# Kernel tuning notes

Hardware: AMD Instinct MI355X
Metric: run time of the kernel (lower is better)

## Reference

```python
import jax, jax.numpy as jnp
import numpy as np

BALL_SIZE = 128


def setup_inputs() -> dict:
    key = jax.random.key(0)
    kq, kk, kv = jax.random.split(key, 3)
    B, H, n, Dh = 4, 16, 8192, 64
    q = jax.random.normal(kq, (B, H, n, Dh), dtype=jnp.float32)
    k = jax.random.normal(kk, (B, H, n, Dh), dtype=jnp.float32)
    v = jax.random.normal(kv, (B, H, n, Dh), dtype=jnp.float32)
    return {"q": q, "k": k, "v": v}


def reference(q, k, v) -> jnp.ndarray:
    # Block-local (ball) attention: attention computed independently within
    # each contiguous ball of size BALL_SIZE along the sequence dim.
    B, H, n, Dh = q.shape
    bs = BALL_SIZE
    m = n // bs
    # (B, H, m, bs, D) -- split seq into balls; attention only within a ball.
    qb = q.reshape(B, H, m, bs, Dh)
    kb = k.reshape(B, H, m, bs, Dh)
    vb = v.reshape(B, H, m, bs, Dh)
    scale = 1.0 / jnp.sqrt(jnp.asarray(Dh, dtype=q.dtype))
    scores = jnp.einsum('bhmqd,bhmkd->bhmqk', qb, kb) * scale  # (B,H,m,bs,bs)
    attn = jax.nn.softmax(scores, axis=-1)
    out = jnp.einsum('bhmqk,bhmkd->bhmqd', attn, vb)
    return out.reshape(B, H, n, Dh)
```

## Files before the change

### kernel.cpp

```cpp
#include <hip/hip_runtime.h>

typedef _Float16 half2_t __attribute__((ext_vector_type(2)));
typedef _Float16 half4_t __attribute__((ext_vector_type(4)));
typedef _Float16 half8_t __attribute__((ext_vector_type(8)));
typedef __fp16   fp16x2  __attribute__((ext_vector_type(2)));
typedef float    f32x4   __attribute__((ext_vector_type(4)));

#define BS 128
#define DH 64

__device__ __forceinline__ half2_t pkrtz(float x, float y) {
  fp16x2 t = __builtin_amdgcn_cvt_pkrtz(x, y);
  return __builtin_bit_cast(half2_t, t);
}

__device__ __forceinline__ half4_t cvt4(const float4 a) {
  half2_t h0 = pkrtz(a.x, a.y);
  half2_t h1 = pkrtz(a.z, a.w);
  return __builtin_shufflevector(h0, h1, 0, 1, 2, 3);
}

__device__ __forceinline__ half8_t cvt8(const float4 a, const float4 b) {
  half2_t h0 = pkrtz(a.x, a.y);
  half2_t h1 = pkrtz(a.z, a.w);
  half2_t h2 = pkrtz(b.x, b.y);
  half2_t h3 = pkrtz(b.z, b.w);
  half4_t lo = __builtin_shufflevector(h0, h1, 0, 1, 2, 3);
  half4_t hi = __builtin_shufflevector(h2, h3, 0, 1, 2, 3);
  return __builtin_shufflevector(lo, hi, 0, 1, 2, 3, 4, 5, 6, 7);
}

__global__ __launch_bounds__(256, 1) void ball_attn_kernel(
    const float* __restrict__ Q, const float* __restrict__ Kk,
    const float* __restrict__ V, float* __restrict__ O) {
  __shared__ __align__(16) _Float16 Kh[BS * DH];
  __shared__ __align__(16) _Float16 VT[DH * BS];
  __shared__ __align__(16) _Float16 Pl[4 * 16 * BS];

  const int tid  = threadIdx.x;
  const int w    = tid >> 6;
  const int lane = tid & 63;
  const int c    = lane & 15;
  const int g    = lane >> 4;

  const size_t base = (size_t)blockIdx.x * (BS * DH);
  const float* Qb = Q + base;
  const float* Kb = Kk + base;
  const float* Vb = V + base;
  float*       Ob = O + base;

  const int d0   = (tid & 15) * 4;
  const int kgrp = tid >> 4;
  float4 vA[4], vB[4], kA[4], kB[4];
#pragma unroll
  for (int it = 0; it < 4; ++it) {
    const int keyA = 2 * kgrp + 32 * it;
    vA[it] = *(const float4*)(Vb + (size_t)keyA * DH + d0);
    vB[it] = *(const float4*)(Vb + (size_t)(keyA + 1) * DH + d0);
    kA[it] = *(const float4*)(Kb + (size_t)keyA * DH + d0);
    kB[it] = *(const float4*)(Kb + (size_t)(keyA + 1) * DH + d0);
  }
#pragma unroll
  for (int it = 0; it < 4; ++it) {
    const int keyA = 2 * kgrp + 32 * it;
    *(half4_t*)&Kh[keyA * DH + (d0 ^ ((keyA & 7) << 3))]           = cvt4(kA[it]);
    *(half4_t*)&Kh[(keyA + 1) * DH + (d0 ^ (((keyA + 1) & 7) << 3))] = cvt4(kB[it]);
    const float* ap = (const float*)&vA[it];
    const float* bp = (const float*)&vB[it];
#pragma unroll
    for (int j = 0; j < 4; ++j) {
      const int d = d0 + j;
      *(half2_t*)&VT[d * BS + (keyA ^ (((d >> 2) & 7) << 3))] = pkrtz(ap[j], bp[j]);
    }
  }

  half8_t aq[2][2];
#pragma unroll
  for (int m = 0; m < 2; ++m)
#pragma unroll
    for (int ks = 0; ks < 2; ++ks) {
      const float* qp = Qb + (w * 32 + m * 16 + c) * DH + ks * 32 + g * 8;
      aq[m][ks] = cvt8(*(const float4*)qp, *(const float4*)(qp + 4));
    }

  __syncthreads();

  f32x4 acc[2][8];
#pragma unroll
  for (int m = 0; m < 2; ++m)
#pragma unroll
    for (int kt = 0; kt < 8; ++kt) acc[m][kt] = (f32x4){0.f, 0.f, 0.f, 0.f};

#pragma unroll
  for (int kt = 0; kt < 8; ++kt)
#pragma unroll
    for (int ks = 0; ks < 2; ++ks) {
      const half8_t bk =
          *(const half8_t*)&Kh[(kt * 16 + c) * DH + ((ks * 32 + g * 8) ^ ((c & 7) << 3))];
      acc[0][kt] = __builtin_amdgcn_mfma_f32_16x16x32_f16(aq[0][ks], bk, acc[0][kt], 0, 0, 0);
      acc[1][kt] = __builtin_amdgcn_mfma_f32_16x16x32_f16(aq[1][ks], bk, acc[1][kt], 0, 0, 0);
    }

#pragma unroll
  for (int m = 0; m < 2; ++m) {
    float mx[4], sm[4], inv[4];
#pragma unroll
    for (int r = 0; r < 4; ++r) {
      mx[r] = acc[m][0][r];
#pragma unroll
      for (int kt = 1; kt < 8; ++kt) mx[r] = fmaxf(mx[r], acc[m][kt][r]);
    }
#pragma unroll
    for (int r = 0; r < 4; ++r) {
      mx[r] = fmaxf(mx[r], __shfl_xor(mx[r], 1));
      mx[r] = fmaxf(mx[r], __shfl_xor(mx[r], 2));
      mx[r] = fmaxf(mx[r], __shfl_xor(mx[r], 4));
      mx[r] = fmaxf(mx[r], __shfl_xor(mx[r], 8));
      sm[r] = 0.f;
    }
#pragma unroll
    for (int kt = 0; kt < 8; ++kt)
#pragma unroll
      for (int r = 0; r < 4; ++r) {
        const float p = __expf((acc[m][kt][r] - mx[r]) * 0.125f);
        acc[m][kt][r] = p;
        sm[r] += p;
      }
#pragma unroll
    for (int r = 0; r < 4; ++r) {
      sm[r] += __shfl_xor(sm[r], 1);
      sm[r] += __shfl_xor(sm[r], 2);
      sm[r] += __shfl_xor(sm[r], 4);
      sm[r] += __shfl_xor(sm[r], 8);
      inv[r] = __builtin_amdgcn_rcpf(sm[r]);
    }
#pragma unroll
    for (int kt = 0; kt < 8; ++kt)
#pragma unroll
      for (int r = 0; r < 4; ++r) {
        const int row = 4 * g + r;
        Pl[(w * 16 + row) * BS + ((kt * 16 + c) ^ ((row & 7) << 3))] =
            (_Float16)acc[m][kt][r];
      }

    f32x4 o[4];
#pragma unroll
    for (int t = 0; t < 4; ++t) o[t] = (f32x4){0.f, 0.f, 0.f, 0.f};
#pragma unroll
    for (int ks = 0; ks < 4; ++ks) {
      const int e0 = ks * 32 + g * 8;
      const half8_t pf = *(const half8_t*)&Pl[(w * 16 + c) * BS + (e0 ^ ((c & 7) << 3))];
#pragma unroll
      for (int t = 0; t < 4; ++t) {
        const int row = t * 16 + c;
        const half8_t vf = *(const half8_t*)&VT[row * BS + (e0 ^ (((row >> 2) & 7) << 3))];
        o[t] = __builtin_amdgcn_mfma_f32_16x16x32_f16(pf, vf, o[t], 0, 0, 0);
      }
    }
#pragma unroll
    for (int t = 0; t < 4; ++t)
#pragma unroll
      for (int r = 0; r < 4; ++r)
        Ob[(w * 32 + m * 16 + 4 * g + r) * DH + t * 16 + c] = o[t][r] * inv[r];
  }
}

extern "C" void kernel_launch(void* const* d_in, const int* in_sizes, int n_in,
                              void* d_out, int out_size, void* d_ws, size_t ws_size,
                              hipStream_t stream) {
  const float* q = (const float*)d_in[0];
  const float* k = (const float*)d_in[1];
  const float* v = (const float*)d_in[2];
  float* out = (float*)d_out;
  const int nballs = in_sizes[0] / (BS * DH);
  ball_attn_kernel<<<dim3(nballs), dim3(256), 0, stream>>>(q, k, v, out);
}
```

Measured before the change: 115.0 us.

## Make ball-attention kernel persistent over 8 balls with async K prefetch

Each block now processes 8 consecutive balls. The next ball's K is prefetched straight into LDS in fp32 via global_load_lds, and V and Q are loaded into registers while the current ball's softmax and PV run. V goes into a double-buffered transposed fp16 tile, and K is converted to fp16 at fragment load time. This hides global-load latency behind compute and changes the V swizzle. The cost is far fewer blocks (512 instead of 4096, fewer than the CU count times occupancy can use), extra syncs and doubled K LDS footprint.

```diff
diff --git a/kernel.cpp b/kernel.cpp
--- a/kernel.cpp
+++ b/kernel.cpp
@@ -8,16 +8,11 @@
 
 #define BS 128
 #define DH 64
+#define NB 8
 
 __device__ __forceinline__ half2_t pkrtz(float x, float y) {
   fp16x2 t = __builtin_amdgcn_cvt_pkrtz(x, y);
   return __builtin_bit_cast(half2_t, t);
-}
-
-__device__ __forceinline__ half4_t cvt4(const float4 a) {
-  half2_t h0 = pkrtz(a.x, a.y);
-  half2_t h1 = pkrtz(a.z, a.w);
-  return __builtin_shufflevector(h0, h1, 0, 1, 2, 3);
 }
 
 __device__ __forceinline__ half8_t cvt8(const float4 a, const float4 b) {
@@ -30,11 +25,13 @@
   return __builtin_shufflevector(lo, hi, 0, 1, 2, 3, 4, 5, 6, 7);
 }
 
+__device__ __forceinline__ int svt(int d) { return (d & 7) ^ ((d >> 2) & 7); }
+
 __global__ __launch_bounds__(256, 1) void ball_attn_kernel(
     const float* __restrict__ Q, const float* __restrict__ Kk,
     const float* __restrict__ V, float* __restrict__ O) {
-  __shared__ __align__(16) _Float16 Kh[BS * DH];
-  __shared__ __align__(16) _Float16 VT[DH * BS];
+  __shared__ __align__(16) float    Kf[BS * DH];
+  __shared__ __align__(16) _Float16 VT2[2][DH * BS];
   __shared__ __align__(16) _Float16 Pl[4 * 16 * BS];
 
   const int tid  = threadIdx.x;
@@ -42,126 +39,242 @@
   const int lane = tid & 63;
   const int c    = lane & 15;
   const int g    = lane >> 4;
-
-  const size_t base = (size_t)blockIdx.x * (BS * DH);
-  const float* Qb = Q + base;
-  const float* Kb = Kk + base;
-  const float* Vb = V + base;
-  float*       Ob = O + base;
-
   const int d0   = (tid & 15) * 4;
   const int kgrp = tid >> 4;
-  float4 vA[4], vB[4], kA[4], kB[4];
-#pragma unroll
-  for (int it = 0; it < 4; ++it) {
-    const int keyA = 2 * kgrp + 32 * it;
-    vA[it] = *(const float4*)(Vb + (size_t)keyA * DH + d0);
-    vB[it] = *(const float4*)(Vb + (size_t)(keyA + 1) * DH + d0);
-    kA[it] = *(const float4*)(Kb + (size_t)keyA * DH + d0);
-    kB[it] = *(const float4*)(Kb + (size_t)(keyA + 1) * DH + d0);
+
+  const size_t ball0 = (size_t)blockIdx.x * NB;
+
+  auto issueK = [&](const float* Kb) {
+#pragma unroll
+    for (int t = 0; t < 8; ++t) {
+      const int row = 32 * w + 4 * t + g;
+      const int u   = (lane & 15) ^ (row & 7);
+      __builtin_amdgcn_global_load_lds(
+          (const __attribute__((address_space(1))) unsigned int*)(Kb + row * DH + u * 4),
+          (__attribute__((address_space(3))) unsigned int*)&Kf[(32 * w + 4 * t) * DH],
+          16, 0, 0);
+    }
+  };
+  auto loadV = [&](const float* Vb, float4* vr) {
+#pragma unroll
+    for (int it = 0; it < 4; ++it) {
+      const int keyA = 2 * kgrp + 32 * it;
+      vr[2 * it]     = *(const float4*)(Vb + (size_t)keyA * DH + d0);
+      vr[2 * it + 1] = *(const float4*)(Vb + (size_t)(keyA + 1) * DH + d0);
+    }
+  };
+  auto writeVT = [&](_Float16* vt, const float4* vr) {
+#pragma unroll
+    for (int it = 0; it < 4; ++it) {
+      const int keyA = 2 * kgrp + 32 * it;
+      const float* ap = (const float*)&vr[2 * it];
+      const float* bp = (const float*)&vr[2 * it + 1];
+#pragma unroll
+      for (int j = 0; j < 4; ++j) {
+        const int d = d0 + j;
+        *(half2_t*)&vt[d * BS + (keyA ^ (svt(d) << 3))] = pkrtz(ap[j], bp[j]);
+      }
+    }
+  };
+  auto loadQ = [&](const float* Qb, float4* qr) {
+#pragma unroll
+    for (int m = 0; m < 2; ++m)
+#pragma unroll
+      for (int ks = 0; ks < 2; ++ks) {
+        const float* qp = Qb + (w * 32 + m * 16 + c) * DH + ks * 32 + g * 8;
+        qr[(m * 2 + ks) * 2]     = *(const float4*)qp;
+        qr[(m * 2 + ks) * 2 + 1] = *(const float4*)(qp + 4);
+      }
+  };
+
+  half8_t aq[2][2];
+  auto cvtQ = [&](const float4* qr) {
+#pragma unroll
+    for (int m = 0; m < 2; ++m)
+#pragma unroll
+      for (int ks = 0; ks < 2; ++ks)
+        aq[m][ks] = cvt8(qr[(m * 2 + ks) * 2], qr[(m * 2 + ks) * 2 + 1]);
+  };
+
+  {
+    const size_t b_off = ball0 * (size_t)(BS * DH);
+    issueK(Kk + b_off);
+    float4 vr[8], qr[8];
+    loadV(V + b_off, vr);
+    loadQ(Q + b_off, qr);
+    cvtQ(qr);
+    writeVT(VT2[0], vr);
+    __syncthreads();
   }
-#pragma unroll
-  for (int it = 0; it < 4; ++it) {
-    const int keyA = 2 * kgrp + 32 * it;
-    *(half4_t*)&Kh[keyA * DH + (d0 ^ ((keyA & 7) << 3))]           = cvt4(kA[it]);
-    *(half4_t*)&Kh[(keyA + 1) * DH + (d0 ^ (((keyA + 1) & 7) << 3))] = cvt4(kB[it]);
-    const float* ap = (const float*)&vA[it];
-    const float* bp = (const float*)&vB[it];
-#pragma unroll
-    for (int j = 0; j < 4; ++j) {
-      const int d = d0 + j;
-      *(half2_t*)&VT[d * BS + (keyA ^ (((d >> 2) & 7) << 3))] = pkrtz(ap[j], bp[j]);
-    }
-  }
-
-  half8_t aq[2][2];
-#pragma unroll
-  for (int m = 0; m < 2; ++m)
-#pragma unroll
-    for (int ks = 0; ks < 2; ++ks) {
-      const float* qp = Qb + (w * 32 + m * 16 + c) * DH + ks * 32 + g * 8;
-      aq[m][ks] = cvt8(*(const float4*)qp, *(const float4*)(qp + 4));
-    }
-
-  __syncthreads();
-
-  f32x4 acc[2][8];
-#pragma unroll
-  for (int m = 0; m < 2; ++m)
-#pragma unroll
-    for (int kt = 0; kt < 8; ++kt) acc[m][kt] = (f32x4){0.f, 0.f, 0.f, 0.f};
-
-#pragma unroll
-  for (int kt = 0; kt < 8; ++kt)
-#pragma unroll
-    for (int ks = 0; ks < 2; ++ks) {
-      const half8_t bk =
-          *(const half8_t*)&Kh[(kt * 16 + c) * DH + ((ks * 32 + g * 8) ^ ((c & 7) << 3))];
-      acc[0][kt] = __builtin_amdgcn_mfma_f32_16x16x32_f16(aq[0][ks], bk, acc[0][kt], 0, 0, 0);
-      acc[1][kt] = __builtin_amdgcn_mfma_f32_16x16x32_f16(aq[1][ks], bk, acc[1][kt], 0, 0, 0);
-    }
-
-#pragma unroll
-  for (int m = 0; m < 2; ++m) {
-    float mx[4], sm[4], inv[4];
-#pragma unroll
-    for (int r = 0; r < 4; ++r) {
-      mx[r] = acc[m][0][r];
-#pragma unroll
-      for (int kt = 1; kt < 8; ++kt) mx[r] = fmaxf(mx[r], acc[m][kt][r]);
-    }
-#pragma unroll
-    for (int r = 0; r < 4; ++r) {
-      mx[r] = fmaxf(mx[r], __shfl_xor(mx[r], 1));
-      mx[r] = fmaxf(mx[r], __shfl_xor(mx[r], 2));
-      mx[r] = fmaxf(mx[r], __shfl_xor(mx[r], 4));
-      mx[r] = fmaxf(mx[r], __shfl_xor(mx[r], 8));
-      sm[r] = 0.f;
-    }
+
+  int cur = 0;
+#pragma unroll 1
+  for (int i = 0; i < NB; ++i) {
+    _Float16* vtcur = VT2[cur];
+    float* Ob = O + (ball0 + i) * (size_t)(BS * DH);
+
+    f32x4 acc[2][8];
+#pragma unroll
+    for (int m = 0; m < 2; ++m)
+#pragma unroll
+      for (int kt = 0; kt < 8; ++kt) acc[m][kt] = (f32x4){0.f, 0.f, 0.f, 0.f};
 #pragma unroll
     for (int kt = 0; kt < 8; ++kt)
 #pragma unroll
-      for (int r = 0; r < 4; ++r) {
-        const float p = __expf((acc[m][kt][r] - mx[r]) * 0.125f);
-        acc[m][kt][r] = p;
-        sm[r] += p;
-      }
-#pragma unroll
-    for (int r = 0; r < 4; ++r) {
-      sm[r] += __shfl_xor(sm[r], 1);
-      sm[r] += __shfl_xor(sm[r], 2);
-      sm[r] += __shfl_xor(sm[r], 4);
-      sm[r] += __shfl_xor(sm[r], 8);
-      inv[r] = __builtin_amdgcn_rcpf(sm[r]);
-    }
-#pragma unroll
-    for (int kt = 0; kt < 8; ++kt)
-#pragma unroll
-      for (int r = 0; r < 4; ++r) {
-        const int row = 4 * g + r;
-        Pl[(w * 16 + row) * BS + ((kt * 16 + c) ^ ((row & 7) << 3))] =
-            (_Float16)acc[m][kt][r];
-      }
-
-    f32x4 o[4];
-#pragma unroll
-    for (int t = 0; t < 4; ++t) o[t] = (f32x4){0.f, 0.f, 0.f, 0.f};
-#pragma unroll
-    for (int ks = 0; ks < 4; ++ks) {
-      const int e0 = ks * 32 + g * 8;
-      const half8_t pf = *(const half8_t*)&Pl[(w * 16 + c) * BS + (e0 ^ ((c & 7) << 3))];
-#pragma unroll
-      for (int t = 0; t < 4; ++t) {
-        const int row = t * 16 + c;
-        const half8_t vf = *(const half8_t*)&VT[row * BS + (e0 ^ (((row >> 2) & 7) << 3))];
-        o[t] = __builtin_amdgcn_mfma_f32_16x16x32_f16(pf, vf, o[t], 0, 0, 0);
-      }
-    }
-#pragma unroll
-    for (int t = 0; t < 4; ++t)
-#pragma unroll
-      for (int r = 0; r < 4; ++r)
-        Ob[(w * 32 + m * 16 + 4 * g + r) * DH + t * 16 + c] = o[t][r] * inv[r];
+      for (int ks = 0; ks < 2; ++ks) {
+        const int row = kt * 16 + c;
+        const int sr  = row & 7;
+        const int u0  = 8 * ks + 2 * g;
+        const float4 a = *(const float4*)&Kf[row * DH + ((u0 ^ sr) * 4)];
+        const float4 b = *(const float4*)&Kf[row * DH + (((u0 + 1) ^ sr) * 4)];
+        const half8_t bk = cvt8(a, b);
+        acc[0][kt] = __builtin_amdgcn_mfma_f32_16x16x32_f16(aq[0][ks], bk, acc[0][kt], 0, 0, 0);
+        acc[1][kt] = __builtin_amdgcn_mfma_f32_16x16x32_f16(aq[1][ks], bk, acc[1][kt], 0, 0, 0);
+      }
+    __syncthreads();
+
+    const bool pf = (i + 1 < NB);
+    const size_t nb_off = (ball0 + i + 1) * (size_t)(BS * DH);
+    if (pf) issueK(Kk + nb_off);
+
+    float4 vraw[8], qraw[8];
+
+    float inv0[4];
+    {
+      float mx[4], sm[4];
+#pragma unroll
+      for (int r = 0; r < 4; ++r) {
+        mx[r] = acc[0][0][r];
+#pragma unroll
+        for (int kt = 1; kt < 8; ++kt) mx[r] = fmaxf(mx[r], acc[0][kt][r]);
+      }
+#pragma unroll
+      for (int r = 0; r < 4; ++r) {
+        mx[r] = fmaxf(mx[r], __shfl_xor(mx[r], 1));
+        mx[r] = fmaxf(mx[r], __shfl_xor(mx[r], 2));
+        mx[r] = fmaxf(mx[r], __shfl_xor(mx[r], 4));
+        mx[r] = fmaxf(mx[r], __shfl_xor(mx[r], 8));
+        sm[r] = 0.f;
+      }
+#pragma unroll
+      for (int kt = 0; kt < 8; ++kt)
+#pragma unroll
+        for (int r = 0; r < 4; ++r) {
+          const float p = __expf((acc[0][kt][r] - mx[r]) * 0.125f);
+          acc[0][kt][r] = p;
+          sm[r] += p;
+        }
+#pragma unroll
+      for (int r = 0; r < 4; ++r) {
+        sm[r] += __shfl_xor(sm[r], 1);
+        sm[r] += __shfl_xor(sm[r], 2);
+        sm[r] += __shfl_xor(sm[r], 4);
+        sm[r] += __shfl_xor(sm[r], 8);
+        inv0[r] = __builtin_amdgcn_rcpf(sm[r]);
+      }
+#pragma unroll
+      for (int kt = 0; kt < 8; ++kt)
+#pragma unroll
+        for (int r = 0; r < 4; ++r) {
+          const int row = 4 * g + r;
+          Pl[(w * 16 + row) * BS + ((kt * 16 + c) ^ ((row & 7) << 3))] =
+              (_Float16)acc[0][kt][r];
+        }
+    }
+    if (pf) loadV(V + nb_off, vraw);
+    {
+      f32x4 o[4];
+#pragma unroll
+      for (int t = 0; t < 4; ++t) o[t] = (f32x4){0.f, 0.f, 0.f, 0.f};
+#pragma unroll
+      for (int ks = 0; ks < 4; ++ks) {
+        const int e0 = ks * 32 + g * 8;
+        const half8_t pfg = *(const half8_t*)&Pl[(w * 16 + c) * BS + (e0 ^ ((c & 7) << 3))];
+#pragma unroll
+        for (int t = 0; t < 4; ++t) {
+          const int rowd = t * 16 + c;
+          const half8_t vf = *(const half8_t*)&vtcur[rowd * BS + (e0 ^ (svt(rowd) << 3))];
+          o[t] = __builtin_amdgcn_mfma_f32_16x16x32_f16(pfg, vf, o[t], 0, 0, 0);
+        }
+      }
+#pragma unroll
+      for (int t = 0; t < 4; ++t)
+#pragma unroll
+        for (int r = 0; r < 4; ++r)
+          Ob[(w * 32 + 4 * g + r) * DH + t * 16 + c] = o[t][r] * inv0[r];
+    }
+
+    float inv1[4];
+    {
+      float mx[4], sm[4];
+#pragma unroll
+      for (int r = 0; r < 4; ++r) {
+        mx[r] = acc[1][0][r];
+#pragma unroll
+        for (int kt = 1; kt < 8; ++kt) mx[r] = fmaxf(mx[r], acc[1][kt][r]);
+      }
+#pragma unroll
+      for (int r = 0; r < 4; ++r) {
+        mx[r] = fmaxf(mx[r], __shfl_xor(mx[r], 1));
+        mx[r] = fmaxf(mx[r], __shfl_xor(mx[r], 2));
+        mx[r] = fmaxf(mx[r], __shfl_xor(mx[r], 4));
+        mx[r] = fmaxf(mx[r], __shfl_xor(mx[r], 8));
+        sm[r] = 0.f;
+      }
+#pragma unroll
+      for (int kt = 0; kt < 8; ++kt)
+#pragma unroll
+        for (int r = 0; r < 4; ++r) {
+          const float p = __expf((acc[1][kt][r] - mx[r]) * 0.125f);
+          acc[1][kt][r] = p;
+          sm[r] += p;
+        }
+#pragma unroll
+      for (int r = 0; r < 4; ++r) {
+        sm[r] += __shfl_xor(sm[r], 1);
+        sm[r] += __shfl_xor(sm[r], 2);
+        sm[r] += __shfl_xor(sm[r], 4);
+        sm[r] += __shfl_xor(sm[r], 8);
+        inv1[r] = __builtin_amdgcn_rcpf(sm[r]);
+      }
+#pragma unroll
+      for (int kt = 0; kt < 8; ++kt)
+#pragma unroll
+        for (int r = 0; r < 4; ++r) {
+          const int row = 4 * g + r;
+          Pl[(w * 16 + row) * BS + ((kt * 16 + c) ^ ((row & 7) << 3))] =
+              (_Float16)acc[1][kt][r];
+        }
+    }
+    if (pf) loadQ(Q + nb_off, qraw);
+    {
+      f32x4 o[4];
+#pragma unroll
+      for (int t = 0; t < 4; ++t) o[t] = (f32x4){0.f, 0.f, 0.f, 0.f};
+#pragma unroll
+      for (int ks = 0; ks < 4; ++ks) {
+        const int e0 = ks * 32 + g * 8;
+        const half8_t pfg = *(const half8_t*)&Pl[(w * 16 + c) * BS + (e0 ^ ((c & 7) << 3))];
+#pragma unroll
+        for (int t = 0; t < 4; ++t) {
+          const int rowd = t * 16 + c;
+          const half8_t vf = *(const half8_t*)&vtcur[rowd * BS + (e0 ^ (svt(rowd) << 3))];
+          o[t] = __builtin_amdgcn_mfma_f32_16x16x32_f16(pfg, vf, o[t], 0, 0, 0);
+        }
+      }
+#pragma unroll
+      for (int t = 0; t < 4; ++t)
+#pragma unroll
+        for (int r = 0; r < 4; ++r)
+          Ob[(w * 32 + 16 + 4 * g + r) * DH + t * 16 + c] = o[t][r] * inv1[r];
+    }
+
+    if (pf) {
+      cvtQ(qraw);
+      writeVT(VT2[cur ^ 1], vraw);
+    }
+    __syncthreads();
+    cur ^= 1;
   }
 }
 
@@ -173,5 +286,5 @@
   const float* v = (const float*)d_in[2];
   float* out = (float*)d_out;
   const int nballs = in_sizes[0] / (BS * DH);
-  ball_attn_kernel<<<dim3(nballs), dim3(256), 0, stream>>>(q, k, v, out);
-}
+  ball_attn_kernel<<<dim3(nballs / NB), dim3(256), 0, stream>>>(q, k, v, out);
+}
```

Measured after the change: 125.7 us. 9.2% more time.

## Stream K fragments from global into registers, drop K LDS staging, remap blocks

Applied to the files above, without the earlier changes.

Removes the shared-memory K buffer. Each wave now loads its K fragments straight from global memory with a two-deep register prefetch and converts them to fp16 just before each MFMA. It also changes the VT swizzle to a new bank-conflict pattern, remaps block IDs to balls in an interleaved order, and drops the one-block-per-SM launch bound so smaller LDS use can allow more resident blocks. The intent is to cut LDS traffic and the staging cost, and to raise occupancy. In exchange, each of the four waves reads all of K from global/L2 separately, which adds redundant global loads.

```diff
diff --git a/kernel.cpp b/kernel.cpp
--- a/kernel.cpp
+++ b/kernel.cpp
@@ -14,12 +14,6 @@
   return __builtin_bit_cast(half2_t, t);
 }
 
-__device__ __forceinline__ half4_t cvt4(const float4 a) {
-  half2_t h0 = pkrtz(a.x, a.y);
-  half2_t h1 = pkrtz(a.z, a.w);
-  return __builtin_shufflevector(h0, h1, 0, 1, 2, 3);
-}
-
 __device__ __forceinline__ half8_t cvt8(const float4 a, const float4 b) {
   half2_t h0 = pkrtz(a.x, a.y);
   half2_t h1 = pkrtz(a.z, a.w);
@@ -30,10 +24,11 @@
   return __builtin_shufflevector(lo, hi, 0, 1, 2, 3, 4, 5, 6, 7);
 }
 
-__global__ __launch_bounds__(256, 1) void ball_attn_kernel(
+__device__ __forceinline__ int svt(int d) { return (d & 7) ^ ((d >> 2) & 7); }
+
+__global__ __launch_bounds__(256) void ball_attn_kernel(
     const float* __restrict__ Q, const float* __restrict__ Kk,
     const float* __restrict__ V, float* __restrict__ O) {
-  __shared__ __align__(16) _Float16 Kh[BS * DH];
   __shared__ __align__(16) _Float16 VT[DH * BS];
   __shared__ __align__(16) _Float16 Pl[4 * 16 * BS];
 
@@ -43,34 +38,36 @@
   const int c    = lane & 15;
   const int g    = lane >> 4;
 
-  const size_t base = (size_t)blockIdx.x * (BS * DH);
+  const int nwg  = gridDim.x;
+  const int bid  = blockIdx.x;
+  const int ball = (bid & 7) * (nwg >> 3) + (bid >> 3);
+
+  const size_t base = (size_t)ball * (BS * DH);
   const float* Qb = Q + base;
   const float* Kb = Kk + base;
   const float* Vb = V + base;
   float*       Ob = O + base;
 
-  const int d0   = (tid & 15) * 4;
-  const int kgrp = tid >> 4;
-  float4 vA[4], vB[4], kA[4], kB[4];
+  {
+    const int kgrp = tid >> 4;
+    const int d0   = (tid & 15) * 4;
+    float4 vA[4], vB[4];
 #pragma unroll
-  for (int it = 0; it < 4; ++it) {
-    const int keyA = 2 * kgrp + 32 * it;
-    vA[it] = *(const float4*)(Vb + (size_t)keyA * DH + d0);
-    vB[it] = *(const float4*)(Vb + (size_t)(keyA + 1) * DH + d0);
-    kA[it] = *(const float4*)(Kb + (size_t)keyA * DH + d0);
-    kB[it] = *(const float4*)(Kb + (size_t)(keyA + 1) * DH + d0);
-  }
+    for (int it = 0; it < 4; ++it) {
+      const int keyA = 2 * kgrp + 32 * it;
+      vA[it] = *(const float4*)(Vb + (size_t)keyA * DH + d0);
+      vB[it] = *(const float4*)(Vb + (size_t)(keyA + 1) * DH + d0);
+    }
 #pragma unroll
-  for (int it = 0; it < 4; ++it) {
-    const int keyA = 2 * kgrp + 32 * it;
-    *(half4_t*)&Kh[keyA * DH + (d0 ^ ((keyA & 7) << 3))]           = cvt4(kA[it]);
-    *(half4_t*)&Kh[(keyA + 1) * DH + (d0 ^ (((keyA + 1) & 7) << 3))] = cvt4(kB[it]);
-    const float* ap = (const float*)&vA[it];
-    const float* bp = (const float*)&vB[it];
+    for (int it = 0; it < 4; ++it) {
+      const int keyA = 2 * kgrp + 32 * it;
+      const float* ap = (const float*)&vA[it];
+      const float* bp = (const float*)&vB[it];
 #pragma unroll
-    for (int j = 0; j < 4; ++j) {
-      const int d = d0 + j;
-      *(half2_t*)&VT[d * BS + (keyA ^ (((d >> 2) & 7) << 3))] = pkrtz(ap[j], bp[j]);
+      for (int j = 0; j < 4; ++j) {
+        const int d = d0 + j;
+        *(half2_t*)&VT[d * BS + (keyA ^ (svt(d) << 3))] = pkrtz(ap[j], bp[j]);
+      }
     }
   }
 
@@ -91,15 +88,28 @@
 #pragma unroll
     for (int kt = 0; kt < 8; ++kt) acc[m][kt] = (f32x4){0.f, 0.f, 0.f, 0.f};
 
+  {
+    float4 kb[2][2];
+    auto kaddr = [&](int i) {
+      const int kt = i >> 1, ks = i & 1;
+      return Kb + (kt * 16 + c) * DH + ks * 32 + g * 8;
+    };
+    kb[0][0] = *(const float4*)kaddr(0);
+    kb[0][1] = *(const float4*)(kaddr(0) + 4);
+    kb[1][0] = *(const float4*)kaddr(1);
+    kb[1][1] = *(const float4*)(kaddr(1) + 4);
 #pragma unroll
-  for (int kt = 0; kt < 8; ++kt)
-#pragma unroll
-    for (int ks = 0; ks < 2; ++ks) {
-      const half8_t bk =
-          *(const half8_t*)&Kh[(kt * 16 + c) * DH + ((ks * 32 + g * 8) ^ ((c & 7) << 3))];
+    for (int i = 0; i < 16; ++i) {
+      const half8_t bk = cvt8(kb[i & 1][0], kb[i & 1][1]);
+      if (i + 2 < 16) {
+        kb[i & 1][0] = *(const float4*)kaddr(i + 2);
+        kb[i & 1][1] = *(const float4*)(kaddr(i + 2) + 4);
+      }
+      const int kt = i >> 1, ks = i & 1;
       acc[0][kt] = __builtin_amdgcn_mfma_f32_16x16x32_f16(aq[0][ks], bk, acc[0][kt], 0, 0, 0);
       acc[1][kt] = __builtin_amdgcn_mfma_f32_16x16x32_f16(aq[1][ks], bk, acc[1][kt], 0, 0, 0);
     }
+  }
 
 #pragma unroll
   for (int m = 0; m < 2; ++m) {
@@ -149,12 +159,12 @@
 #pragma unroll
     for (int ks = 0; ks < 4; ++ks) {
       const int e0 = ks * 32 + g * 8;
-      const half8_t pf = *(const half8_t*)&Pl[(w * 16 + c) * BS + (e0 ^ ((c & 7) << 3))];
+      const half8_t pfg = *(const half8_t*)&Pl[(w * 16 + c) * BS + (e0 ^ ((c & 7) << 3))];
 #pragma unroll
       for (int t = 0; t < 4; ++t) {
-        const int row = t * 16 + c;
-        const half8_t vf = *(const half8_t*)&VT[row * BS + (e0 ^ (((row >> 2) & 7) << 3))];
-        o[t] = __builtin_amdgcn_mfma_f32_16x16x32_f16(pf, vf, o[t], 0, 0, 0);
+        const int rowd = t * 16 + c;
+        const half8_t vf = *(const half8_t*)&VT[rowd * BS + (e0 ^ (svt(rowd) << 3))];
+        o[t] = __builtin_amdgcn_mfma_f32_16x16x32_f16(pfg, vf, o[t], 0, 0, 0);
       }
     }
 #pragma unroll
```

Result: slower. 131.6 us (+14.4%).

## Switch to 32x32 MFMA with transposed scores and register-resident P

Applied to the files above, without the earlier changes.

Recomputes S^T = K·Q^T using 32x32x16 MFMA so each lane holds a full query column, which lets the softmax reductions run within a lane plus one cross-half shuffle. K is read straight from global into MFMA operands, so the K shared-memory tile is gone. The P matrix is repacked in registers with permlane32 swaps instead of going through LDS. V^T staging uses a new swizzle and the launch-bounds occupancy hint is removed. The aim is to cut LDS traffic, LDS footprint and shuffle count. In exchange, each wave now loads K from global/L2 on its own, four times per block, and register pressure rises.

```diff
diff --git a/kernel.cpp b/kernel.cpp
--- a/kernel.cpp
+++ b/kernel.cpp
@@ -4,23 +4,21 @@
 typedef _Float16 half4_t __attribute__((ext_vector_type(4)));
 typedef _Float16 half8_t __attribute__((ext_vector_type(8)));
 typedef __fp16   fp16x2  __attribute__((ext_vector_type(2)));
-typedef float    f32x4   __attribute__((ext_vector_type(4)));
+typedef float    f32x16  __attribute__((ext_vector_type(16)));
 
 #define BS 128
 #define DH 64
 
-__device__ __forceinline__ half2_t pkrtz(float x, float y) {
+static __device__ __forceinline__ half2_t pkrtz(float x, float y) {
   fp16x2 t = __builtin_amdgcn_cvt_pkrtz(x, y);
   return __builtin_bit_cast(half2_t, t);
 }
-
-__device__ __forceinline__ half4_t cvt4(const float4 a) {
-  half2_t h0 = pkrtz(a.x, a.y);
-  half2_t h1 = pkrtz(a.z, a.w);
-  return __builtin_shufflevector(h0, h1, 0, 1, 2, 3);
+static __device__ __forceinline__ unsigned pkrtz_u(float x, float y) {
+  fp16x2 t = __builtin_amdgcn_cvt_pkrtz(x, y);
+  return __builtin_bit_cast(unsigned, t);
 }
 
-__device__ __forceinline__ half8_t cvt8(const float4 a, const float4 b) {
+static __device__ __forceinline__ half8_t cvt8(const float4 a, const float4 b) {
   half2_t h0 = pkrtz(a.x, a.y);
   half2_t h1 = pkrtz(a.z, a.w);
   half2_t h2 = pkrtz(b.x, b.y);
@@ -30,18 +28,46 @@
   return __builtin_shufflevector(lo, hi, 0, 1, 2, 3, 4, 5, 6, 7);
 }
 
-__global__ __launch_bounds__(256, 1) void ball_attn_kernel(
+static __device__ __forceinline__ half8_t h8_from(unsigned r0, unsigned r1,
+                                                  unsigned r2, unsigned r3) {
+  half2_t h0 = __builtin_bit_cast(half2_t, r0);
+  half2_t h1 = __builtin_bit_cast(half2_t, r1);
+  half2_t h2 = __builtin_bit_cast(half2_t, r2);
+  half2_t h3 = __builtin_bit_cast(half2_t, r3);
+  half4_t lo = __builtin_shufflevector(h0, h1, 0, 1, 2, 3);
+  half4_t hi = __builtin_shufflevector(h2, h3, 0, 1, 2, 3);
+  return __builtin_shufflevector(lo, hi, 0, 1, 2, 3, 4, 5, 6, 7);
+}
+
+static __device__ __forceinline__ void plswap(unsigned x, unsigned y,
+                                              unsigned& olo, unsigned& ohi) {
+#if __has_builtin(__builtin_amdgcn_permlane32_swap)
+  auto pr = __builtin_amdgcn_permlane32_swap((int)x, (int)y, false, false);
+  unsigned tmp[2];
+  __builtin_memcpy(tmp, &pr, 8);
+  olo = tmp[0];
+  ohi = tmp[1];
+#else
+  const int h = (threadIdx.x & 63) >> 5;
+  unsigned xs = (unsigned)__shfl_xor((int)x, 32);
+  unsigned ys = (unsigned)__shfl_xor((int)y, 32);
+  olo = h ? ys : x;
+  ohi = h ? y : xs;
+#endif
+}
+
+static __device__ __forceinline__ int svt(int d) { return (d & 7) ^ ((d >> 2) & 7); }
+
+__global__ __launch_bounds__(256) void ball_attn_kernel(
     const float* __restrict__ Q, const float* __restrict__ Kk,
     const float* __restrict__ V, float* __restrict__ O) {
-  __shared__ __align__(16) _Float16 Kh[BS * DH];
   __shared__ __align__(16) _Float16 VT[DH * BS];
-  __shared__ __align__(16) _Float16 Pl[4 * 16 * BS];
 
   const int tid  = threadIdx.x;
   const int w    = tid >> 6;
   const int lane = tid & 63;
-  const int c    = lane & 15;
-  const int g    = lane >> 4;
+  const int ld   = lane & 31;
+  const int hi   = lane >> 5;
 
   const size_t base = (size_t)blockIdx.x * (BS * DH);
   const float* Qb = Q + base;
@@ -49,120 +75,104 @@
   const float* Vb = V + base;
   float*       Ob = O + base;
 
-  const int d0   = (tid & 15) * 4;
-  const int kgrp = tid >> 4;
-  float4 vA[4], vB[4], kA[4], kB[4];
+  {
+    const int kgrp = tid >> 4;
+    const int d0   = (tid & 15) * 4;
+    float4 vA[4], vB[4];
 #pragma unroll
-  for (int it = 0; it < 4; ++it) {
-    const int keyA = 2 * kgrp + 32 * it;
-    vA[it] = *(const float4*)(Vb + (size_t)keyA * DH + d0);
-    vB[it] = *(const float4*)(Vb + (size_t)(keyA + 1) * DH + d0);
-    kA[it] = *(const float4*)(Kb + (size_t)keyA * DH + d0);
-    kB[it] = *(const float4*)(Kb + (size_t)(keyA + 1) * DH + d0);
-  }
+    for (int it = 0; it < 4; ++it) {
+      const int keyA = 2 * kgrp + 32 * it;
+      vA[it] = *(const float4*)(Vb + (size_t)keyA * DH + d0);
+      vB[it] = *(const float4*)(Vb + (size_t)(keyA + 1) * DH + d0);
+    }
 #pragma unroll
-  for (int it = 0; it < 4; ++it) {
-    const int keyA = 2 * kgrp + 32 * it;
-    *(half4_t*)&Kh[keyA * DH + (d0 ^ ((keyA & 7) << 3))]           = cvt4(kA[it]);
-    *(half4_t*)&Kh[(keyA + 1) * DH + (d0 ^ (((keyA + 1) & 7) << 3))] = cvt4(kB[it]);
-    const float* ap = (const float*)&vA[it];
-    const float* bp = (const float*)&vB[it];
+    for (int it = 0; it < 4; ++it) {
+      const int keyA = 2 * kgrp + 32 * it;
+      const float* ap = (const float*)&vA[it];
+      const float* bp = (const float*)&vB[it];
 #pragma unroll
-    for (int j = 0; j < 4; ++j) {
-      const int d = d0 + j;
-      *(half2_t*)&VT[d * BS + (keyA ^ (((d >> 2) & 7) << 3))] = pkrtz(ap[j], bp[j]);
+      for (int j = 0; j < 4; ++j) {
+        const int d = d0 + j;
+        *(half2_t*)&VT[d * BS + (keyA ^ (svt(d) << 3))] = pkrtz(ap[j], bp[j]);
+      }
     }
   }
 
-  half8_t aq[2][2];
+  half8_t bq[4];
 #pragma unroll
-  for (int m = 0; m < 2; ++m)
-#pragma unroll
-    for (int ks = 0; ks < 2; ++ks) {
-      const float* qp = Qb + (w * 32 + m * 16 + c) * DH + ks * 32 + g * 8;
-      aq[m][ks] = cvt8(*(const float4*)qp, *(const float4*)(qp + 4));
-    }
+  for (int dstep = 0; dstep < 4; ++dstep) {
+    const float* qp = Qb + (w * 32 + ld) * DH + dstep * 16 + hi * 8;
+    bq[dstep] = cvt8(*(const float4*)qp, *(const float4*)(qp + 4));
+  }
 
   __syncthreads();
 
-  f32x4 acc[2][8];
+  f32x16 acc[4] = {};
 #pragma unroll
-  for (int m = 0; m < 2; ++m)
+  for (int kt = 0; kt < 4; ++kt) {
+    const float* krow = Kb + (kt * 32 + ld) * DH + hi * 8;
 #pragma unroll
-    for (int kt = 0; kt < 8; ++kt) acc[m][kt] = (f32x4){0.f, 0.f, 0.f, 0.f};
+    for (int dstep = 0; dstep < 4; ++dstep) {
+      const float* kp = krow + dstep * 16;
+      const half8_t ak = cvt8(*(const float4*)kp, *(const float4*)(kp + 4));
+      acc[kt] = __builtin_amdgcn_mfma_f32_32x32x16_f16(ak, bq[dstep], acc[kt], 0, 0, 0);
+    }
+  }
+
+  float mx = acc[0][0];
+#pragma unroll
+  for (int kt = 0; kt < 4; ++kt)
+#pragma unroll
+    for (int r = 0; r < 16; ++r) mx = fmaxf(mx, acc[kt][r]);
+  mx = fmaxf(mx, __shfl_xor(mx, 32));
+  const float nmxs = -mx * 0.125f;
+  float sm = 0.f;
+#pragma unroll
+  for (int kt = 0; kt < 4; ++kt)
+#pragma unroll
+    for (int r = 0; r < 16; ++r) {
+      const float p = __expf(fmaf(acc[kt][r], 0.125f, nmxs));
+      acc[kt][r] = p;
+      sm += p;
+    }
+  sm += __shfl_xor(sm, 32);
+  const float inv = __builtin_amdgcn_rcpf(sm);
+
+  half8_t pf[8];
+#pragma unroll
+  for (int s = 0; s < 8; ++s) {
+    const int kt = s >> 1;
+    const int bA = 2 * (s & 1);
+    const int bB = bA + 1;
+    const unsigned A0 = pkrtz_u(acc[kt][4 * bA + 0] * inv, acc[kt][4 * bA + 1] * inv);
+    const unsigned A1 = pkrtz_u(acc[kt][4 * bA + 2] * inv, acc[kt][4 * bA + 3] * inv);
+    const unsigned B0 = pkrtz_u(acc[kt][4 * bB + 0] * inv, acc[kt][4 * bB + 1] * inv);
+    const unsigned B1 = pkrtz_u(acc[kt][4 * bB + 2] * inv, acc[kt][4 * bB + 3] * inv);
+    unsigned r0, r1, r2, r3;
+    plswap(A0, B0, r0, r2);
+    plswap(A1, B1, r1, r3);
+    pf[s] = h8_from(r0, r1, r2, r3);
+  }
+
+  f32x16 o[2] = {};
+#pragma unroll
+  for (int dt = 0; dt < 2; ++dt) {
+    const int row = dt * 32 + ld;
+    const int sv  = svt(row) << 3;
+#pragma unroll
+    for (int s = 0; s < 8; ++s) {
+      const half8_t vf = *(const half8_t*)&VT[row * BS + ((16 * s + 8 * hi) ^ sv)];
+      o[dt] = __builtin_amdgcn_mfma_f32_32x32x16_f16(pf[s], vf, o[dt], 0, 0, 0);
+    }
+  }
 
 #pragma unroll
-  for (int kt = 0; kt < 8; ++kt)
+  for (int dt = 0; dt < 2; ++dt)
 #pragma unroll
-    for (int ks = 0; ks < 2; ++ks) {
-      const half8_t bk =
-          *(const half8_t*)&Kh[(kt * 16 + c) * DH + ((ks * 32 + g * 8) ^ ((c & 7) << 3))];
-      acc[0][kt] = __builtin_amdgcn_mfma_f32_16x16x32_f16(aq[0][ks], bk, acc[0][kt], 0, 0, 0);
-      acc[1][kt] = __builtin_amdgcn_mfma_f32_16x16x32_f16(aq[1][ks], bk, acc[1][kt], 0, 0, 0);
+    for (int r = 0; r < 16; ++r) {
+      const int qrow = w * 32 + (r & 3) + 8 * (r >> 2) + 4 * hi;
+      Ob[qrow * DH + dt * 32 + ld] = o[dt][r];
     }
-
-#pragma unroll
-  for (int m = 0; m < 2; ++m) {
-    float mx[4], sm[4], inv[4];
-#pragma unroll
-    for (int r = 0; r < 4; ++r) {
-      mx[r] = acc[m][0][r];
-#pragma unroll
-      for (int kt = 1; kt < 8; ++kt) mx[r] = fmaxf(mx[r], acc[m][kt][r]);
-    }
-#pragma unroll
-    for (int r = 0; r < 4; ++r) {
-      mx[r] = fmaxf(mx[r], __shfl_xor(mx[r], 1));
-      mx[r] = fmaxf(mx[r], __shfl_xor(mx[r], 2));
-      mx[r] = fmaxf(mx[r], __shfl_xor(mx[r], 4));
-      mx[r] = fmaxf(mx[r], __shfl_xor(mx[r], 8));
-      sm[r] = 0.f;
-    }
-#pragma unroll
-    for (int kt = 0; kt < 8; ++kt)
-#pragma unroll
-      for (int r = 0; r < 4; ++r) {
-        const float p = __expf((acc[m][kt][r] - mx[r]) * 0.125f);
-        acc[m][kt][r] = p;
-        sm[r] += p;
-      }
-#pragma unroll
-    for (int r = 0; r < 4; ++r) {
-      sm[r] += __shfl_xor(sm[r], 1);
-      sm[r] += __shfl_xor(sm[r], 2);
-      sm[r] += __shfl_xor(sm[r], 4);
-      sm[r] += __shfl_xor(sm[r], 8);
-      inv[r] = __builtin_amdgcn_rcpf(sm[r]);
-    }
-#pragma unroll
-    for (int kt = 0; kt < 8; ++kt)
-#pragma unroll
-      for (int r = 0; r < 4; ++r) {
-        const int row = 4 * g + r;
-        Pl[(w * 16 + row) * BS + ((kt * 16 + c) ^ ((row & 7) << 3))] =
-            (_Float16)acc[m][kt][r];
-      }
-
-    f32x4 o[4];
-#pragma unroll
-    for (int t = 0; t < 4; ++t) o[t] = (f32x4){0.f, 0.f, 0.f, 0.f};
-#pragma unroll
-    for (int ks = 0; ks < 4; ++ks) {
-      const int e0 = ks * 32 + g * 8;
-      const half8_t pf = *(const half8_t*)&Pl[(w * 16 + c) * BS + (e0 ^ ((c & 7) << 3))];
-#pragma unroll
-      for (int t = 0; t < 4; ++t) {
-        const int row = t * 16 + c;
-        const half8_t vf = *(const half8_t*)&VT[row * BS + (e0 ^ (((row >> 2) & 7) << 3))];
-        o[t] = __builtin_amdgcn_mfma_f32_16x16x32_f16(pf, vf, o[t], 0, 0, 0);
-      }
-    }
-#pragma unroll
-    for (int t = 0; t < 4; ++t)
-#pragma unroll
-      for (int r = 0; r < 4; ++r)
-        Ob[(w * 32 + m * 16 + 4 * g + r) * DH + t * 16 + c] = o[t][r] * inv[r];
-  }
 }
 
 extern "C" void kernel_launch(void* const* d_in, const int* in_sizes, int n_in,
```

New measurement: 140.2 us. +21.9%, slower.
